# Kernel optimization log

Measured on AMD Instinct MI355X. Metric: run time of the kernel, lower is better.

## Reference

```python
import jax, jax.numpy as jnp
import numpy as np

EPS = 1e-08  # attention offset, matches module epsilon


def _ln(x, g, b, eps=1e-5):
    m = jnp.mean(x, axis=-1, keepdims=True)
    v = jnp.var(x, axis=-1, keepdims=True)
    return (x - m) * jax.lax.rsqrt(v + eps) * g + b


def setup_inputs() -> dict:
    key = jax.random.key(0)
    ks = jax.random.split(key, 12)
    B, N, D, S, H = 32, 16384, 64, 7, 128
    sc = 1.0 / np.sqrt(D)
    sch = 1.0 / np.sqrt(H)
    return {
        "inputs": jax.random.normal(ks[0], (B, N, D), jnp.float32),
        "ln_in_g": jnp.ones((D,), jnp.float32), "ln_in_b": jnp.zeros((D,), jnp.float32),
        "ln_slots_g": jnp.ones((D,), jnp.float32), "ln_slots_b": jnp.zeros((D,), jnp.float32),
        "ln_mlp_g": jnp.ones((D,), jnp.float32), "ln_mlp_b": jnp.zeros((D,), jnp.float32),
        "Wq": jax.random.normal(ks[1], (D, D), jnp.float32) * sc,
        "Wk": jax.random.normal(ks[2], (D, D), jnp.float32) * sc,
        "Wv": jax.random.normal(ks[3], (D, D), jnp.float32) * sc,
        "slots_mu": jax.random.normal(ks[4], (1, 1, D), jnp.float32),
        "slots_log_sigma": jax.random.normal(ks[5], (1, 1, D), jnp.float32) * 0.1,
        "w_ih": jax.random.normal(ks[6], (3 * D, D), jnp.float32) * sc,
        "w_hh": jax.random.normal(ks[7], (3 * D, D), jnp.float32) * sc,
        "b_ih": jnp.zeros((3 * D,), jnp.float32), "b_hh": jnp.zeros((3 * D,), jnp.float32),
        "mlp_w1": jax.random.normal(ks[8], (H, D), jnp.float32) * sc,
        "mlp_b1": jnp.zeros((H,), jnp.float32),
        "mlp_w2": jax.random.normal(ks[9], (D, H), jnp.float32) * sch,
        "mlp_b2": jnp.zeros((D,), jnp.float32),
        "noise_slots": jax.random.normal(ks[10], (B, S, D), jnp.float32),
        "noise_h": jax.random.normal(ks[11], (B, D), jnp.float32),
        "num_iterations": 3,
    }


def reference(inputs, ln_in_g, ln_in_b, ln_slots_g, ln_slots_b, ln_mlp_g, ln_mlp_b,
              Wq, Wk, Wv, slots_mu, slots_log_sigma, w_ih, w_hh, b_ih, b_hh,
              mlp_w1, mlp_b1, mlp_w2, mlp_b2, noise_slots, noise_h, num_iterations):
    D = inputs.shape[-1]
    scale = D ** -0.5

    x = _ln(inputs, ln_in_g, ln_in_b)               # [B,N,D]
    k = jnp.einsum('bnd,ed->bne', x, Wk)            # [B,N,D]
    v = jnp.einsum('bnd,ed->bne', x, Wv)            # [B,N,D]

    sigma = jnp.exp(slots_log_sigma)
    slots = slots_mu + sigma * noise_slots          # [B,S,D]
    h0 = (slots_mu + sigma * noise_h[None])[0]      # [B,D] (torch h0 is [1,B,D])

    def gru_step(h, x_t):  # torch GRU cell, gate order r,z,n
        gi = x_t @ w_ih.T + b_ih
        gh = h @ w_hh.T + b_hh
        ir, iz, inn = jnp.split(gi, 3, axis=-1)
        hr, hz, hn = jnp.split(gh, 3, axis=-1)
        r = jax.nn.sigmoid(ir + hr)
        z = jax.nn.sigmoid(iz + hz)
        n = jnp.tanh(inn + r * hn)
        h_new = (1.0 - z) * n + z * h
        return h_new, h_new

    for _ in range(num_iterations):
        sn = _ln(slots, ln_slots_g, ln_slots_b)
        q = jnp.einsum('bsd,ed->bse', sn, Wq) * scale        # [B,S,D]
        logits = jnp.einsum('bnd,bsd->bns', k, q)            # [B,N,S]
        attn = jax.nn.softmax(logits, axis=-1) + EPS          # softmax over slots
        attn = attn / jnp.sum(attn, axis=1, keepdims=True)   # normalize over inputs (dim=-2)
        updates = jnp.einsum('bns,bnd->bsd', attn, v)        # [B,S,D]
        # nn.GRU over the slot axis as "time", fixed h0 each iteration
        _, hs = jax.lax.scan(gru_step, h0, jnp.swapaxes(updates, 0, 1))
        slots = jnp.swapaxes(hs, 0, 1)                       # [B,S,D]
        hid = jax.nn.relu(_ln(slots, ln_mlp_g, ln_mlp_b) @ mlp_w1.T + mlp_b1)
        slots = slots + (hid @ mlp_w2.T + mlp_b2)
    return slots
```

## Files before the change

### kernel.cpp

```cpp
#include <hip/hip_runtime.h>
#include <hip/hip_bf16.h>


#define B_ 32
#define N_ 16384
#define D_ 64
#define S_ 7

typedef __bf16 bf16x8 __attribute__((ext_vector_type(8)));
typedef float floatx4 __attribute__((ext_vector_type(4)));

__device__ __forceinline__ unsigned int f2bfu(float f) {
  __hip_bfloat16 h = __float2bfloat16(f);
  return (unsigned int)__builtin_bit_cast(unsigned short, h);
}
__device__ __forceinline__ unsigned int pack2bf(float lo, float hi) {
  return f2bfu(lo) | (f2bfu(hi) << 16);
}

__device__ void q_from_slots(const float* s_slot, float* s_tmp,
                             const float* __restrict__ g, const float* __restrict__ bb,
                             const float* __restrict__ Wq, float* __restrict__ qout,
                             int lane, int w)
{
  for (int ss = 0; ss < 2; ++ss) {
    int srow = ss * 4 + w;
    if (srow < 7) {
      float xv = s_slot[srow * 64 + lane];
      float s1 = xv, s2 = xv * xv;
#pragma unroll
      for (int mm = 1; mm < 64; mm <<= 1) {
        s1 += __shfl_xor(s1, mm);
        s2 += __shfl_xor(s2, mm);
      }
      float mean = s1 * 0.015625f;
      float var = s2 * 0.015625f - mean * mean;
      float rs = rsqrtf(var + 1e-5f);
      s_tmp[w * 64 + lane] = (xv - mean) * rs * g[lane] + bb[lane];
    }
    __syncthreads();
    if (srow < 7) {
      float acc = 0.f;
      const float4* wr = (const float4*)(Wq + lane * 64);
      const float4* xr = (const float4*)(s_tmp + w * 64);
#pragma unroll
      for (int i = 0; i < 16; ++i) {
        float4 a = wr[i], xx = xr[i];
        acc += a.x * xx.x + a.y * xx.y + a.z * xx.z + a.w * xx.w;
      }
      qout[srow * 64 + lane] = acc * 0.125f;
    }
    __syncthreads();
  }
}

__global__ __launch_bounds__(256) void init_kernel(
    const float* __restrict__ mu, const float* __restrict__ lsig,
    const float* __restrict__ nslots, const float* __restrict__ nh,
    const float* __restrict__ ln_s_g, const float* __restrict__ ln_s_b,
    const float* __restrict__ Wq,
    const float* __restrict__ Wk, const float* __restrict__ Wv,
    float* __restrict__ qbuf, float* __restrict__ h0b,
    unsigned short* __restrict__ wkb, unsigned short* __restrict__ wvb)
{
  __shared__ float s_slot[448];
  __shared__ float s_tmp[256];
  const int b = blockIdx.x, t = threadIdx.x, lane = t & 63, w = t >> 6;
  {
    int gid = b * 256 + t;
    if (gid < 4096) wkb[gid] = (unsigned short)f2bfu(Wk[gid]);
    else            wvb[gid - 4096] = (unsigned short)f2bfu(Wv[gid - 4096]);
  }
  for (int o = t; o < 448; o += 256) {
    int d = o & 63;
    s_slot[o] = mu[d] + expf(lsig[d]) * nslots[b * 448 + o];
  }
  if (t < 64) h0b[b * 64 + t] = mu[t] + expf(lsig[t]) * nh[b * 64 + t];
  __syncthreads();
  q_from_slots(s_slot, s_tmp, ln_s_g, ln_s_b, Wq, qbuf + b * 448, lane, w);
}

__global__ __launch_bounds__(256, 4) void proj_kernel(
    const float* __restrict__ x,
    const float* __restrict__ lng, const float* __restrict__ lnb,
    const unsigned short* __restrict__ wkb, const unsigned short* __restrict__ wvb,
    const float* __restrict__ qbuf,
    unsigned short* __restrict__ kb, unsigned short* __restrict__ vt,
    float* __restrict__ Wp, float* __restrict__ Cp)
{
  __shared__ __align__(16) unsigned char smemA[18432];
  __shared__ __align__(16) unsigned short s_vo[64 * 136];
  __shared__ __align__(16) unsigned short s_qb[1024];
  __shared__ float s_cred[4][8];
  unsigned short* s_xn = (unsigned short*)smemA;
  unsigned short* s_ko = (unsigned short*)smemA;
  unsigned short* s_at = (unsigned short*)smemA;
  float* s_red = (float*)(smemA + 5120);

  const int t = threadIdx.x, lane = t & 63, w = t >> 6;
  const int R0 = blockIdx.x * 128;
  const int bb = R0 >> 14;
  const int tile = blockIdx.x;

  {
    int i0 = t * 4;
    int s = i0 >> 6, d0 = i0 & 63;
    float f0 = 0.f, f1 = 0.f, f2 = 0.f, f3 = 0.f;
    if (s < 7) {
      const float* qp = qbuf + bb * 448 + s * 64 + d0;
      f0 = qp[0]; f1 = qp[1]; f2 = qp[2]; f3 = qp[3];
    }
    uint2 p;
    p.x = pack2bf(f0, f1);
    p.y = pack2bf(f2, f3);
    *(uint2*)&s_qb[i0] = p;
  }

  const int ql = t & 3;
  float4 g4[4], b4[4];
#pragma unroll
  for (int j = 0; j < 4; ++j) {
    g4[j] = *(const float4*)&lng[ql * 16 + j * 4];
    b4[j] = *(const float4*)&lnb[ql * 16 + j * 4];
  }
#pragma unroll
  for (int half = 0; half < 2; ++half) {
    int r = half * 64 + (t >> 2);
    const float4* xp = (const float4*)&x[(size_t)(R0 + r) * 64 + ql * 16];
    float4 xv[4];
#pragma unroll
    for (int j = 0; j < 4; ++j) xv[j] = xp[j];
    float s1 = 0.f, s2 = 0.f;
#pragma unroll
    for (int j = 0; j < 4; ++j) {
      s1 += xv[j].x + xv[j].y + xv[j].z + xv[j].w;
      s2 += xv[j].x * xv[j].x + xv[j].y * xv[j].y + xv[j].z * xv[j].z + xv[j].w * xv[j].w;
    }
    s1 += __shfl_xor(s1, 1); s2 += __shfl_xor(s2, 1);
    s1 += __shfl_xor(s1, 2); s2 += __shfl_xor(s2, 2);
    float mean = s1 * 0.015625f;
    float var = s2 * 0.015625f - mean * mean;
    float rs = rsqrtf(var + 1e-5f);
    float y[16];
#pragma unroll
    for (int j = 0; j < 4; ++j) {
      y[j * 4 + 0] = (xv[j].x - mean) * rs * g4[j].x + b4[j].x;
      y[j * 4 + 1] = (xv[j].y - mean) * rs * g4[j].y + b4[j].y;
      y[j * 4 + 2] = (xv[j].z - mean) * rs * g4[j].z + b4[j].z;
      y[j * 4 + 3] = (xv[j].w - mean) * rs * g4[j].w + b4[j].w;
    }
#pragma unroll
    for (int h = 0; h < 2; ++h) {
      uint4 p;
      p.x = pack2bf(y[h * 8 + 0], y[h * 8 + 1]);
      p.y = pack2bf(y[h * 8 + 2], y[h * 8 + 3]);
      p.z = pack2bf(y[h * 8 + 4], y[h * 8 + 5]);
      p.w = pack2bf(y[h * 8 + 6], y[h * 8 + 7]);
      int c = ql * 2 + h;
      int sc = c ^ (r & 7);
      *(uint4*)&s_xn[r * 64 + sc * 8] = p;
    }
  }
  __syncthreads();

  const int m16 = lane & 15, quad = lane >> 4;
  bf16x8 bq0 = *(const bf16x8*)&s_qb[m16 * 64 + quad * 8];
  bf16x8 bq1 = *(const bf16x8*)&s_qb[m16 * 64 + 32 + quad * 8];

  bf16x8 bf[2][2];
#pragma unroll
  for (int rt = 0; rt < 2; ++rt) {
    int xr = (w * 2 + rt) * 16 + m16;
#pragma unroll
    for (int kk = 0; kk < 2; ++kk)
      bf[rt][kk] = *(const bf16x8*)&s_xn[xr * 64 + (((kk * 4 + quad) ^ (xr & 7)) * 8)];
  }
  bf16x8 wkf[4][2], wvf[4][2];
#pragma unroll
  for (int ft = 0; ft < 4; ++ft)
#pragma unroll
    for (int kk = 0; kk < 2; ++kk) {
      wkf[ft][kk] = *(const bf16x8*)&wkb[(ft * 16 + m16) * 64 + kk * 32 + quad * 8];
      wvf[ft][kk] = *(const bf16x8*)&wvb[(ft * 16 + m16) * 64 + kk * 32 + quad * 8];
    }
  __syncthreads();

#pragma unroll
  for (int ft = 0; ft < 4; ++ft)
#pragma unroll
    for (int rt = 0; rt < 2; ++rt) {
      floatx4 acc = (floatx4){0.f, 0.f, 0.f, 0.f};
      acc = __builtin_amdgcn_mfma_f32_16x16x32_bf16(wkf[ft][0], bf[rt][0], acc, 0, 0, 0);
      acc = __builtin_amdgcn_mfma_f32_16x16x32_bf16(wkf[ft][1], bf[rt][1], acc, 0, 0, 0);
      int n_l = (w * 2 + rt) * 16 + m16;
      uint2 p;
      p.x = pack2bf(acc[0], acc[1]);
      p.y = pack2bf(acc[2], acc[3]);
      *(uint2*)&s_ko[n_l * 72 + ft * 16 + quad * 4] = p;
    }
  __syncthreads();

#pragma unroll
  for (int ft = 0; ft < 4; ++ft)
#pragma unroll
    for (int rt = 0; rt < 2; ++rt) {
      floatx4 acc = (floatx4){0.f, 0.f, 0.f, 0.f};
      acc = __builtin_amdgcn_mfma_f32_16x16x32_bf16(bf[rt][0], wvf[ft][0], acc, 0, 0, 0);
      acc = __builtin_amdgcn_mfma_f32_16x16x32_bf16(bf[rt][1], wvf[ft][1], acc, 0, 0, 0);
      int n_l = (w * 2 + rt) * 16 + quad * 4;
      int d0 = ft * 16 + m16;
      uint2 p;
      p.x = pack2bf(acc[0], acc[1]);
      p.y = pack2bf(acc[2], acc[3]);
      *(uint2*)&s_vo[d0 * 136 + n_l] = p;
    }
  bf16x8 ak[2][2];
#pragma unroll
  for (int rt = 0; rt < 2; ++rt) {
    int row = (w * 2 + rt) * 16 + m16;
    ak[rt][0] = *(const bf16x8*)&s_ko[row * 72 + quad * 8];
    ak[rt][1] = *(const bf16x8*)&s_ko[row * 72 + 32 + quad * 8];
  }
#pragma unroll
  for (int p = 0; p < 4; ++p) {
    int ii = (p * 256 + t) * 8;
    int n_l = ii >> 6, dl = ii & 63;
    uint4 v4 = *(const uint4*)&s_ko[n_l * 72 + dl];
    *(uint4*)&kb[(size_t)(R0 + n_l) * 64 + dl] = v4;
  }
  __syncthreads();

  float cl = 0.f;
#pragma unroll
  for (int rt = 0; rt < 2; ++rt) {
    floatx4 c = (floatx4){0.f, 0.f, 0.f, 0.f};
    c = __builtin_amdgcn_mfma_f32_16x16x32_bf16(ak[rt][0], bq0, c, 0, 0, 0);
    c = __builtin_amdgcn_mfma_f32_16x16x32_bf16(ak[rt][1], bq1, c, 0, 0, 0);
    float atv[4];
#pragma unroll
    for (int rg = 0; rg < 4; ++rg) {
      float e = (m16 < 7) ? __expf(c[rg]) : 0.f;
      float sm = e;
      sm += __shfl_xor(sm, 1);
      sm += __shfl_xor(sm, 2);
      sm += __shfl_xor(sm, 4);
      float a = e * __builtin_amdgcn_rcpf(sm) + 1e-8f;
      atv[rg] = a;
      cl += a;
    }
    if (m16 < 7) {
      uint2 p;
      p.x = pack2bf(atv[0], atv[1]);
      p.y = pack2bf(atv[2], atv[3]);
      *(uint2*)&s_at[w * 640 + m16 * 40 + rt * 16 + quad * 4] = p;
    }
  }
  asm volatile("s_waitcnt lgkmcnt(0)" ::: "memory");
  bf16x8 af = *(const bf16x8*)&s_at[w * 640 + m16 * 40 + quad * 8];
  floatx4 acc2[4];
#pragma unroll
  for (int dt = 0; dt < 4; ++dt) acc2[dt] = (floatx4){0.f, 0.f, 0.f, 0.f};
#pragma unroll
  for (int dt = 0; dt < 4; ++dt) {
    bf16x8 bv = *(const bf16x8*)&s_vo[(dt * 16 + m16) * 136 + w * 32 + quad * 8];
    acc2[dt] = __builtin_amdgcn_mfma_f32_16x16x32_bf16(af, bv, acc2[dt], 0, 0, 0);
  }
  if (quad < 2) {
#pragma unroll
    for (int dt = 0; dt < 4; ++dt)
#pragma unroll
      for (int rg = 0; rg < 4; ++rg) {
        int s = quad * 4 + rg;
        if (s < 7) s_red[w * 448 + s * 64 + dt * 16 + m16] = acc2[dt][rg];
      }
  }
  cl += __shfl_xor(cl, 16);
  cl += __shfl_xor(cl, 32);
  if (m16 < 7 && quad == 0) s_cred[w][m16] = cl;
  __syncthreads();

  for (int o = t; o < 448; o += 256) {
    float v = s_red[o] + s_red[448 + o] + s_red[896 + o] + s_red[1344 + o];
    Wp[(size_t)tile * 448 + o] = v;
  }
  if (t < 7) {
    float c = s_cred[0][t] + s_cred[1][t] + s_cred[2][t] + s_cred[3][t];
    Cp[(size_t)tile * 8 + t] = c;
  }
#pragma unroll
  for (int p = 0; p < 4; ++p) {
    int ii = (p * 256 + t) * 8;
    int d0 = ii >> 7, nl = ii & 127;
    uint4 v4 = *(const uint4*)&s_vo[d0 * 136 + nl];
    *(uint4*)&vt[(size_t)tile * 8192 + ii] = v4;
  }
}

__global__ __launch_bounds__(256, 4) void attn_kernel(
    const unsigned short* __restrict__ kb, const unsigned short* __restrict__ vt,
    const float* __restrict__ qbuf,
    float* __restrict__ Wp, float* __restrict__ Cp)
{
  __shared__ __align__(16) unsigned short s_qb[16 * 64];
  __shared__ __align__(16) unsigned short s_at[4][16 * 72];
  __shared__ __align__(16) float s_red[4][448];
  __shared__ float s_cred[4][8];

  const int b = blockIdx.y;
  const int t = threadIdx.x, lane = t & 63, w = t >> 6;
  const int m16 = lane & 15, quad = lane >> 4;

  {
    int i0 = t * 4;
    int s = i0 >> 6, d0 = i0 & 63;
    float f0 = 0.f, f1 = 0.f, f2 = 0.f, f3 = 0.f;
    if (s < 7) {
      const float* qp = qbuf + b * 448 + s * 64 + d0;
      f0 = qp[0]; f1 = qp[1]; f2 = qp[2]; f3 = qp[3];
    }
    uint2 p;
    p.x = pack2bf(f0, f1);
    p.y = pack2bf(f2, f3);
    *(uint2*)&s_qb[i0] = p;
  }
  __syncthreads();

  bf16x8 bq0 = *(const bf16x8*)&s_qb[m16 * 64 + quad * 8];
  bf16x8 bq1 = *(const bf16x8*)&s_qb[m16 * 64 + 32 + quad * 8];

  const int n0w = blockIdx.x * 256 + w * 64;
  const unsigned short* kbA = kb + ((size_t)b * N_ + n0w) * 64;

  bf16x8 ak[4][2];
#pragma unroll
  for (int nt = 0; nt < 4; ++nt) {
    ak[nt][0] = *(const bf16x8*)&kbA[(size_t)(nt * 16 + m16) * 64 + quad * 8];
    ak[nt][1] = *(const bf16x8*)&kbA[(size_t)(nt * 16 + m16) * 64 + 32 + quad * 8];
  }
  floatx4 cc[4];
#pragma unroll
  for (int nt = 0; nt < 4; ++nt) {
    floatx4 c = (floatx4){0.f, 0.f, 0.f, 0.f};
    c = __builtin_amdgcn_mfma_f32_16x16x32_bf16(ak[nt][0], bq0, c, 0, 0, 0);
    c = __builtin_amdgcn_mfma_f32_16x16x32_bf16(ak[nt][1], bq1, c, 0, 0, 0);
    cc[nt] = c;
  }
  float cl = 0.f;
#pragma unroll
  for (int nt = 0; nt < 4; ++nt) {
    float atv[4];
#pragma unroll
    for (int rg = 0; rg < 4; ++rg) {
      float e = (m16 < 7) ? __expf(cc[nt][rg]) : 0.f;
      float sm = e;
      sm += __shfl_xor(sm, 1);
      sm += __shfl_xor(sm, 2);
      sm += __shfl_xor(sm, 4);
      float a = e * __builtin_amdgcn_rcpf(sm) + 1e-8f;
      atv[rg] = a;
      cl += a;
    }
    if (m16 < 7) {
      uint2 p;
      p.x = pack2bf(atv[0], atv[1]);
      p.y = pack2bf(atv[2], atv[3]);
      *(uint2*)&s_at[w][m16 * 72 + nt * 16 + quad * 4] = p;
    }
  }

  bf16x8 bv[2][4];
  const unsigned short* vtB = vt + (size_t)(b * 128 + (n0w >> 7)) * 8192 + (n0w & 127);
#pragma unroll
  for (int ch = 0; ch < 2; ++ch)
#pragma unroll
    for (int dt = 0; dt < 4; ++dt)
      bv[ch][dt] = *(const bf16x8*)&vtB[(dt * 16 + m16) * 128 + ch * 32 + quad * 8];
  asm volatile("s_waitcnt lgkmcnt(0)" ::: "memory");
  bf16x8 af0 = *(const bf16x8*)&s_at[w][m16 * 72 + quad * 8];
  bf16x8 af1 = *(const bf16x8*)&s_at[w][m16 * 72 + 32 + quad * 8];

  floatx4 acc[4];
#pragma unroll
  for (int dt = 0; dt < 4; ++dt) acc[dt] = (floatx4){0.f, 0.f, 0.f, 0.f};
#pragma unroll
  for (int dt = 0; dt < 4; ++dt)
    acc[dt] = __builtin_amdgcn_mfma_f32_16x16x32_bf16(af0, bv[0][dt], acc[dt], 0, 0, 0);
#pragma unroll
  for (int dt = 0; dt < 4; ++dt)
    acc[dt] = __builtin_amdgcn_mfma_f32_16x16x32_bf16(af1, bv[1][dt], acc[dt], 0, 0, 0);

  if (quad < 2) {
#pragma unroll
    for (int dt = 0; dt < 4; ++dt)
#pragma unroll
      for (int rg = 0; rg < 4; ++rg) {
        int s = quad * 4 + rg;
        if (s < 7) s_red[w][s * 64 + dt * 16 + m16] = acc[dt][rg];
      }
  }
  cl += __shfl_xor(cl, 16);
  cl += __shfl_xor(cl, 32);
  if (m16 < 7 && quad == 0) s_cred[w][m16] = cl;
  __syncthreads();

  for (int o = t; o < 448; o += 256) {
    float v = s_red[0][o] + s_red[1][o] + s_red[2][o] + s_red[3][o];
    Wp[((size_t)b * 64 + blockIdx.x) * 448 + o] = v;
  }
  if (t < 7) {
    float c = s_cred[0][t] + s_cred[1][t] + s_cred[2][t] + s_cred[3][t];
    Cp[((size_t)b * 64 + blockIdx.x) * 8 + t] = c;
  }
}

__global__ __launch_bounds__(512) void slot_update_kernel(
    const float* __restrict__ Wp, const float* __restrict__ Cp, int npart,
    const float* __restrict__ h0b,
    const float* __restrict__ w_ih, const float* __restrict__ w_hh,
    const float* __restrict__ b_ih, const float* __restrict__ b_hh,
    const float* __restrict__ ln_m_g, const float* __restrict__ ln_m_b,
    const float* __restrict__ w1, const float* __restrict__ b1,
    const float* __restrict__ w2, const float* __restrict__ b2,
    const float* __restrict__ ln_s_g, const float* __restrict__ ln_s_b,
    const float* __restrict__ Wq,
    float* __restrict__ qbuf, float* __restrict__ out, int flags)
{
  const int b = blockIdx.x, t = threadIdx.x, lane = t & 63, w = t >> 6;
  __shared__ float s_whhT[64 * 201];
  __shared__ float s_upd[448];
  __shared__ float s_gi[1344];
  __shared__ float s_slot[448];
  __shared__ float s_tmp[512];
  __shared__ float s_cs[8];

  for (int i = t; i < 12288; i += 512) {
    int j = i >> 6, d = i & 63;
    s_whhT[d * 201 + j] = w_hh[i];
  }
  if (t < 7) {
    float cs = 0.f;
#pragma unroll 8
    for (int p = 0; p < npart; ++p) cs += Cp[((size_t)b * npart + p) * 8 + t];
    s_cs[t] = cs;
  }
  __syncthreads();
  if (t < 448) {
    float acc = 0.f;
#pragma unroll 8
    for (int p = 0; p < npart; ++p) acc += Wp[((size_t)b * npart + p) * 448 + t];
    s_upd[t] = acc / s_cs[t >> 6];
  }
  __syncthreads();
  for (int o = t; o < 1344; o += 512) {
    int s = o / 192, j = o - s * 192;
    float acc = b_ih[j];
    const float4* wr = (const float4*)(w_ih + j * 64);
    const float4* ur = (const float4*)(s_upd + s * 64);
#pragma unroll
    for (int i = 0; i < 16; ++i) {
      float4 a = wr[i], u = ur[i];
      acc += a.x * u.x + a.y * u.y + a.z * u.z + a.w * u.w;
    }
    s_gi[o] = acc;
  }
  __syncthreads();
  if (w == 0) {
    float h = h0b[b * 64 + lane];
    const float bhr = b_hh[lane], bhz = b_hh[64 + lane], bhn = b_hh[128 + lane];
    const float* wr_ = &s_whhT[lane];
    const float* wz_ = &s_whhT[64 + lane];
    const float* wn_ = &s_whhT[128 + lane];
    for (int s = 0; s < 7; ++s) {
      float ar = bhr, az = bhz, an = bhn;
#pragma unroll 8
      for (int d = 0; d < 64; ++d) {
        float hd = __shfl(h, d);
        ar += hd * wr_[d * 201];
        az += hd * wz_[d * 201];
        an += hd * wn_[d * 201];
      }
      float ir = s_gi[s * 192 + lane], iz = s_gi[s * 192 + 64 + lane], inn = s_gi[s * 192 + 128 + lane];
      float r = 1.f / (1.f + __expf(-(ir + ar)));
      float z = 1.f / (1.f + __expf(-(iz + az)));
      float n = tanhf(inn + r * an);
      h = (1.f - z) * n + z * h;
      s_slot[s * 64 + lane] = h;
    }
  }
  __syncthreads();
  float* s_sn = s_gi;
  float* s_hid = s_gi + 448;
  if (w < 7) {
    float xv = s_slot[w * 64 + lane];
    float s1 = xv, s2 = xv * xv;
#pragma unroll
    for (int mm = 1; mm < 64; mm <<= 1) {
      s1 += __shfl_xor(s1, mm);
      s2 += __shfl_xor(s2, mm);
    }
    float mean = s1 * 0.015625f;
    float var = s2 * 0.015625f - mean * mean;
    float rs = rsqrtf(var + 1e-5f);
    s_sn[w * 64 + lane] = (xv - mean) * rs * ln_m_g[lane] + ln_m_b[lane];
  }
  __syncthreads();
  for (int o = t; o < 896; o += 512) {
    int s = o >> 7, hh = o & 127;
    float acc = b1[hh];
    const float4* wr = (const float4*)(w1 + hh * 64);
    const float4* xr = (const float4*)(s_sn + s * 64);
#pragma unroll
    for (int i = 0; i < 16; ++i) {
      float4 a = wr[i], xx = xr[i];
      acc += a.x * xx.x + a.y * xx.y + a.z * xx.z + a.w * xx.w;
    }
    s_hid[o] = fmaxf(acc, 0.f);
  }
  __syncthreads();
  for (int o = t; o < 448; o += 512) {
    int s = o >> 6, d = o & 63;
    float acc = b2[d];
    const float4* wr = (const float4*)(w2 + d * 128);
    const float4* hr = (const float4*)(s_hid + s * 128);
#pragma unroll
    for (int i = 0; i < 32; ++i) {
      float4 a = wr[i], hv = hr[i];
      acc += a.x * hv.x + a.y * hv.y + a.z * hv.z + a.w * hv.w;
    }
    float val = s_slot[o] + acc;
    s_slot[o] = val;
    if (flags & 1) out[b * 448 + o] = val;
  }
  __syncthreads();
  if (flags & 2) {
    if (w < 7) {
      float xv = s_slot[w * 64 + lane];
      float s1 = xv, s2 = xv * xv;
#pragma unroll
      for (int mm = 1; mm < 64; mm <<= 1) {
        s1 += __shfl_xor(s1, mm);
        s2 += __shfl_xor(s2, mm);
      }
      float mean = s1 * 0.015625f;
      float var = s2 * 0.015625f - mean * mean;
      float rs = rsqrtf(var + 1e-5f);
      s_tmp[w * 64 + lane] = (xv - mean) * rs * ln_s_g[lane] + ln_s_b[lane];
    }
    __syncthreads();
    if (w < 7) {
      float acc = 0.f;
      const float4* wr = (const float4*)(Wq + lane * 64);
      const float4* xr = (const float4*)(s_tmp + w * 64);
#pragma unroll
      for (int i = 0; i < 16; ++i) {
        float4 a = wr[i], xx = xr[i];
        acc += a.x * xx.x + a.y * xx.y + a.z * xx.z + a.w * xx.w;
      }
      qbuf[b * 448 + w * 64 + lane] = acc * 0.125f;
    }
  }
}

extern "C" void kernel_launch(void* const* d_in, const int* in_sizes, int n_in,
                              void* d_out, int out_size, void* d_ws, size_t ws_size,
                              hipStream_t stream)
{
  (void)in_sizes; (void)n_in; (void)out_size; (void)ws_size;
  const float* x      = (const float*)d_in[0];
  const float* ln_in_g = (const float*)d_in[1];
  const float* ln_in_b = (const float*)d_in[2];
  const float* ln_s_g  = (const float*)d_in[3];
  const float* ln_s_b  = (const float*)d_in[4];
  const float* ln_m_g  = (const float*)d_in[5];
  const float* ln_m_b  = (const float*)d_in[6];
  const float* Wq = (const float*)d_in[7];
  const float* Wk = (const float*)d_in[8];
  const float* Wv = (const float*)d_in[9];
  const float* mu = (const float*)d_in[10];
  const float* lsig = (const float*)d_in[11];
  const float* w_ih = (const float*)d_in[12];
  const float* w_hh = (const float*)d_in[13];
  const float* b_ih = (const float*)d_in[14];
  const float* b_hh = (const float*)d_in[15];
  const float* w1 = (const float*)d_in[16];
  const float* b1 = (const float*)d_in[17];
  const float* w2 = (const float*)d_in[18];
  const float* b2 = (const float*)d_in[19];
  const float* nslots = (const float*)d_in[20];
  const float* nh = (const float*)d_in[21];

  unsigned short* kb  = (unsigned short*)d_ws;
  unsigned short* vt  = kb + (size_t)B_ * N_ * D_;
  unsigned short* wkb = vt + (size_t)B_ * N_ * D_;
  unsigned short* wvb = wkb + 4096;
  float* fb  = (float*)(wvb + 4096);
  float* qbuf = fb;
  float* h0b  = fb + 14336;
  float* Wp   = fb + 16384;
  float* Cp   = Wp + 1835008;
  float* out = (float*)d_out;

  init_kernel<<<32, 256, 0, stream>>>(mu, lsig, nslots, nh, ln_s_g, ln_s_b, Wq,
                                      Wk, Wv, qbuf, h0b, wkb, wvb);
  proj_kernel<<<4096, 256, 0, stream>>>(x, ln_in_g, ln_in_b, wkb, wvb, qbuf, kb, vt, Wp, Cp);
  slot_update_kernel<<<32, 512, 0, stream>>>(Wp, Cp, 128, h0b, w_ih, w_hh, b_ih, b_hh,
                                             ln_m_g, ln_m_b, w1, b1, w2, b2,
                                             ln_s_g, ln_s_b, Wq, qbuf, out, 2);
  attn_kernel<<<dim3(64, 32), 256, 0, stream>>>(kb, vt, qbuf, Wp, Cp);
  slot_update_kernel<<<32, 512, 0, stream>>>(Wp, Cp, 64, h0b, w_ih, w_hh, b_ih, b_hh,
                                             ln_m_g, ln_m_b, w1, b1, w2, b2,
                                             ln_s_g, ln_s_b, Wq, qbuf, out, 2);
  attn_kernel<<<dim3(64, 32), 256, 0, stream>>>(kb, vt, qbuf, Wp, Cp);
  slot_update_kernel<<<32, 512, 0, stream>>>(Wp, Cp, 64, h0b, w_ih, w_hh, b_ih, b_hh,
                                             ln_m_g, ln_m_b, w1, b1, w2, b2,
                                             ln_s_g, ln_s_b, Wq, qbuf, out, 1);
}
```

Before: 449.5 us.

## Fuse iterations 2-3 attention and slot updates into one per-batch persistent kernel

Replaces the separate attention and slot-update launches for the later iterations with a single kernel that uses one 1024-thread block per batch. Each block streams its batch's K and V tiles, computes attention with MFMA, reduces in shared memory and runs the GRU and MLP update in place, keeping q in shared memory. The GRU hidden-weight product now reads w_hh directly from global memory instead of staging a transpose in LDS. This removes launch and global round-trip overhead but restricts the bandwidth-heavy attention passes to only 32 workgroups.

```diff
diff --git a/kernel.cpp b/kernel.cpp
--- a/kernel.cpp
+++ b/kernel.cpp
@@ -84,7 +84,7 @@
     const float* __restrict__ x,
     const float* __restrict__ lng, const float* __restrict__ lnb,
     const unsigned short* __restrict__ wkb, const unsigned short* __restrict__ wvb,
-    const float* __restrict__ qbuf,
+    const float* __restrict__ qin,
     unsigned short* __restrict__ kb, unsigned short* __restrict__ vt,
     float* __restrict__ Wp, float* __restrict__ Cp)
 {
@@ -107,7 +107,7 @@
     int s = i0 >> 6, d0 = i0 & 63;
     float f0 = 0.f, f1 = 0.f, f2 = 0.f, f3 = 0.f;
     if (s < 7) {
-      const float* qp = qbuf + bb * 448 + s * 64 + d0;
+      const float* qp = qin + bb * 448 + s * 64 + d0;
       f0 = qp[0]; f1 = qp[1]; f2 = qp[2]; f3 = qp[3];
     }
     uint2 p;
@@ -290,131 +290,14 @@
 #pragma unroll
   for (int p = 0; p < 4; ++p) {
     int ii = (p * 256 + t) * 8;
-    int d0 = ii >> 7, nl = ii & 127;
-    uint4 v4 = *(const uint4*)&s_vo[d0 * 136 + nl];
+    uint4 v4 = *(const uint4*)&s_vo[(ii >> 7) * 136 + (ii & 127)];
     *(uint4*)&vt[(size_t)tile * 8192 + ii] = v4;
   }
 }
 
-__global__ __launch_bounds__(256, 4) void attn_kernel(
-    const unsigned short* __restrict__ kb, const unsigned short* __restrict__ vt,
-    const float* __restrict__ qbuf,
-    float* __restrict__ Wp, float* __restrict__ Cp)
-{
-  __shared__ __align__(16) unsigned short s_qb[16 * 64];
-  __shared__ __align__(16) unsigned short s_at[4][16 * 72];
-  __shared__ __align__(16) float s_red[4][448];
-  __shared__ float s_cred[4][8];
-
-  const int b = blockIdx.y;
-  const int t = threadIdx.x, lane = t & 63, w = t >> 6;
-  const int m16 = lane & 15, quad = lane >> 4;
-
-  {
-    int i0 = t * 4;
-    int s = i0 >> 6, d0 = i0 & 63;
-    float f0 = 0.f, f1 = 0.f, f2 = 0.f, f3 = 0.f;
-    if (s < 7) {
-      const float* qp = qbuf + b * 448 + s * 64 + d0;
-      f0 = qp[0]; f1 = qp[1]; f2 = qp[2]; f3 = qp[3];
-    }
-    uint2 p;
-    p.x = pack2bf(f0, f1);
-    p.y = pack2bf(f2, f3);
-    *(uint2*)&s_qb[i0] = p;
-  }
-  __syncthreads();
-
-  bf16x8 bq0 = *(const bf16x8*)&s_qb[m16 * 64 + quad * 8];
-  bf16x8 bq1 = *(const bf16x8*)&s_qb[m16 * 64 + 32 + quad * 8];
-
-  const int n0w = blockIdx.x * 256 + w * 64;
-  const unsigned short* kbA = kb + ((size_t)b * N_ + n0w) * 64;
-
-  bf16x8 ak[4][2];
-#pragma unroll
-  for (int nt = 0; nt < 4; ++nt) {
-    ak[nt][0] = *(const bf16x8*)&kbA[(size_t)(nt * 16 + m16) * 64 + quad * 8];
-    ak[nt][1] = *(const bf16x8*)&kbA[(size_t)(nt * 16 + m16) * 64 + 32 + quad * 8];
-  }
-  floatx4 cc[4];
-#pragma unroll
-  for (int nt = 0; nt < 4; ++nt) {
-    floatx4 c = (floatx4){0.f, 0.f, 0.f, 0.f};
-    c = __builtin_amdgcn_mfma_f32_16x16x32_bf16(ak[nt][0], bq0, c, 0, 0, 0);
-    c = __builtin_amdgcn_mfma_f32_16x16x32_bf16(ak[nt][1], bq1, c, 0, 0, 0);
-    cc[nt] = c;
-  }
-  float cl = 0.f;
-#pragma unroll
-  for (int nt = 0; nt < 4; ++nt) {
-    float atv[4];
-#pragma unroll
-    for (int rg = 0; rg < 4; ++rg) {
-      float e = (m16 < 7) ? __expf(cc[nt][rg]) : 0.f;
-      float sm = e;
-      sm += __shfl_xor(sm, 1);
-      sm += __shfl_xor(sm, 2);
-      sm += __shfl_xor(sm, 4);
-      float a = e * __builtin_amdgcn_rcpf(sm) + 1e-8f;
-      atv[rg] = a;
-      cl += a;
-    }
-    if (m16 < 7) {
-      uint2 p;
-      p.x = pack2bf(atv[0], atv[1]);
-      p.y = pack2bf(atv[2], atv[3]);
-      *(uint2*)&s_at[w][m16 * 72 + nt * 16 + quad * 4] = p;
-    }
-  }
-
-  bf16x8 bv[2][4];
-  const unsigned short* vtB = vt + (size_t)(b * 128 + (n0w >> 7)) * 8192 + (n0w & 127);
-#pragma unroll
-  for (int ch = 0; ch < 2; ++ch)
-#pragma unroll
-    for (int dt = 0; dt < 4; ++dt)
-      bv[ch][dt] = *(const bf16x8*)&vtB[(dt * 16 + m16) * 128 + ch * 32 + quad * 8];
-  asm volatile("s_waitcnt lgkmcnt(0)" ::: "memory");
-  bf16x8 af0 = *(const bf16x8*)&s_at[w][m16 * 72 + quad * 8];
-  bf16x8 af1 = *(const bf16x8*)&s_at[w][m16 * 72 + 32 + quad * 8];
-
-  floatx4 acc[4];
-#pragma unroll
-  for (int dt = 0; dt < 4; ++dt) acc[dt] = (floatx4){0.f, 0.f, 0.f, 0.f};
-#pragma unroll
-  for (int dt = 0; dt < 4; ++dt)
-    acc[dt] = __builtin_amdgcn_mfma_f32_16x16x32_bf16(af0, bv[0][dt], acc[dt], 0, 0, 0);
-#pragma unroll
-  for (int dt = 0; dt < 4; ++dt)
-    acc[dt] = __builtin_amdgcn_mfma_f32_16x16x32_bf16(af1, bv[1][dt], acc[dt], 0, 0, 0);
-
-  if (quad < 2) {
-#pragma unroll
-    for (int dt = 0; dt < 4; ++dt)
-#pragma unroll
-      for (int rg = 0; rg < 4; ++rg) {
-        int s = quad * 4 + rg;
-        if (s < 7) s_red[w][s * 64 + dt * 16 + m16] = acc[dt][rg];
-      }
-  }
-  cl += __shfl_xor(cl, 16);
-  cl += __shfl_xor(cl, 32);
-  if (m16 < 7 && quad == 0) s_cred[w][m16] = cl;
-  __syncthreads();
-
-  for (int o = t; o < 448; o += 256) {
-    float v = s_red[0][o] + s_red[1][o] + s_red[2][o] + s_red[3][o];
-    Wp[((size_t)b * 64 + blockIdx.x) * 448 + o] = v;
-  }
-  if (t < 7) {
-    float c = s_cred[0][t] + s_cred[1][t] + s_cred[2][t] + s_cred[3][t];
-    Cp[((size_t)b * 64 + blockIdx.x) * 8 + t] = c;
-  }
-}
-
-__global__ __launch_bounds__(512) void slot_update_kernel(
-    const float* __restrict__ Wp, const float* __restrict__ Cp, int npart,
+__device__ void slot_core_1024(
+    int b, int t, int lane, int w,
+    float* s_upd, float* s_gi, float* s_slot, unsigned short* s_qb,
     const float* __restrict__ h0b,
     const float* __restrict__ w_ih, const float* __restrict__ w_hh,
     const float* __restrict__ b_ih, const float* __restrict__ b_hh,
@@ -423,35 +306,10 @@
     const float* __restrict__ w2, const float* __restrict__ b2,
     const float* __restrict__ ln_s_g, const float* __restrict__ ln_s_b,
     const float* __restrict__ Wq,
-    float* __restrict__ qbuf, float* __restrict__ out, int flags)
+    float* __restrict__ out, int flags)
 {
-  const int b = blockIdx.x, t = threadIdx.x, lane = t & 63, w = t >> 6;
-  __shared__ float s_whhT[64 * 201];
-  __shared__ float s_upd[448];
-  __shared__ float s_gi[1344];
-  __shared__ float s_slot[448];
-  __shared__ float s_tmp[512];
-  __shared__ float s_cs[8];
-
-  for (int i = t; i < 12288; i += 512) {
-    int j = i >> 6, d = i & 63;
-    s_whhT[d * 201 + j] = w_hh[i];
-  }
-  if (t < 7) {
-    float cs = 0.f;
-#pragma unroll 8
-    for (int p = 0; p < npart; ++p) cs += Cp[((size_t)b * npart + p) * 8 + t];
-    s_cs[t] = cs;
-  }
-  __syncthreads();
-  if (t < 448) {
-    float acc = 0.f;
-#pragma unroll 8
-    for (int p = 0; p < npart; ++p) acc += Wp[((size_t)b * npart + p) * 448 + t];
-    s_upd[t] = acc / s_cs[t >> 6];
-  }
-  __syncthreads();
-  for (int o = t; o < 1344; o += 512) {
+  __syncthreads();
+  for (int o = t; o < 1344; o += 1024) {
     int s = o / 192, j = o - s * 192;
     float acc = b_ih[j];
     const float4* wr = (const float4*)(w_ih + j * 64);
@@ -467,17 +325,19 @@
   if (w == 0) {
     float h = h0b[b * 64 + lane];
     const float bhr = b_hh[lane], bhz = b_hh[64 + lane], bhn = b_hh[128 + lane];
-    const float* wr_ = &s_whhT[lane];
-    const float* wz_ = &s_whhT[64 + lane];
-    const float* wn_ = &s_whhT[128 + lane];
+    const float4* wr4 = (const float4*)(w_hh + lane * 64);
+    const float4* wz4 = (const float4*)(w_hh + (64 + lane) * 64);
+    const float4* wn4 = (const float4*)(w_hh + (128 + lane) * 64);
     for (int s = 0; s < 7; ++s) {
       float ar = bhr, az = bhz, an = bhn;
-#pragma unroll 8
-      for (int d = 0; d < 64; ++d) {
-        float hd = __shfl(h, d);
-        ar += hd * wr_[d * 201];
-        az += hd * wz_[d * 201];
-        an += hd * wn_[d * 201];
+#pragma unroll
+      for (int i = 0; i < 16; ++i) {
+        float4 a = wr4[i], zz = wz4[i], c = wn4[i];
+        float h0 = __shfl(h, i * 4 + 0), h1 = __shfl(h, i * 4 + 1);
+        float h2 = __shfl(h, i * 4 + 2), h3 = __shfl(h, i * 4 + 3);
+        ar += a.x * h0 + a.y * h1 + a.z * h2 + a.w * h3;
+        az += zz.x * h0 + zz.y * h1 + zz.z * h2 + zz.w * h3;
+        an += c.x * h0 + c.y * h1 + c.z * h2 + c.w * h3;
       }
       float ir = s_gi[s * 192 + lane], iz = s_gi[s * 192 + 64 + lane], inn = s_gi[s * 192 + 128 + lane];
       float r = 1.f / (1.f + __expf(-(ir + ar)));
@@ -504,7 +364,7 @@
     s_sn[w * 64 + lane] = (xv - mean) * rs * ln_m_g[lane] + ln_m_b[lane];
   }
   __syncthreads();
-  for (int o = t; o < 896; o += 512) {
+  for (int o = t; o < 896; o += 1024) {
     int s = o >> 7, hh = o & 127;
     float acc = b1[hh];
     const float4* wr = (const float4*)(w1 + hh * 64);
@@ -517,7 +377,7 @@
     s_hid[o] = fmaxf(acc, 0.f);
   }
   __syncthreads();
-  for (int o = t; o < 448; o += 512) {
+  for (int o = t; o < 448; o += 1024) {
     int s = o >> 6, d = o & 63;
     float acc = b2[d];
     const float4* wr = (const float4*)(w2 + d * 128);
@@ -544,20 +404,164 @@
       float mean = s1 * 0.015625f;
       float var = s2 * 0.015625f - mean * mean;
       float rs = rsqrtf(var + 1e-5f);
-      s_tmp[w * 64 + lane] = (xv - mean) * rs * ln_s_g[lane] + ln_s_b[lane];
+      s_upd[w * 64 + lane] = (xv - mean) * rs * ln_s_g[lane] + ln_s_b[lane];
     }
     __syncthreads();
     if (w < 7) {
       float acc = 0.f;
       const float4* wr = (const float4*)(Wq + lane * 64);
-      const float4* xr = (const float4*)(s_tmp + w * 64);
+      const float4* xr = (const float4*)(s_upd + w * 64);
 #pragma unroll
       for (int i = 0; i < 16; ++i) {
         float4 a = wr[i], xx = xr[i];
         acc += a.x * xx.x + a.y * xx.y + a.z * xx.z + a.w * xx.w;
       }
-      qbuf[b * 448 + w * 64 + lane] = acc * 0.125f;
-    }
+      s_qb[w * 64 + lane] = (unsigned short)f2bfu(acc * 0.125f);
+    }
+  }
+}
+
+__global__ __launch_bounds__(1024) void iter23_kernel(
+    const unsigned short* __restrict__ kb, const unsigned short* __restrict__ vt,
+    const float* __restrict__ Wp, const float* __restrict__ Cp,
+    const float* __restrict__ h0b,
+    const float* __restrict__ w_ih, const float* __restrict__ w_hh,
+    const float* __restrict__ b_ih, const float* __restrict__ b_hh,
+    const float* __restrict__ ln_m_g, const float* __restrict__ ln_m_b,
+    const float* __restrict__ w1, const float* __restrict__ b1,
+    const float* __restrict__ w2, const float* __restrict__ b2,
+    const float* __restrict__ ln_s_g, const float* __restrict__ ln_s_b,
+    const float* __restrict__ Wq,
+    float* __restrict__ out)
+{
+  __shared__ __align__(16) unsigned short s_qb[1024];
+  __shared__ __align__(16) unsigned short s_at[16][1152];
+  __shared__ __align__(16) float s_red[16][448];
+  __shared__ float s_cred[16][8];
+  __shared__ float s_upd[448];
+  __shared__ float s_gi[1344];
+  __shared__ float s_slot[448];
+  __shared__ float s_cs[8];
+
+  const int b = blockIdx.x;
+  const int t = threadIdx.x, lane = t & 63, w = t >> 6;
+  const int m16 = lane & 15, quad = lane >> 4;
+
+  s_qb[t] = 0;
+
+  {
+    if (t < 7) {
+      float cs = 0.f;
+#pragma unroll 8
+      for (int p = 0; p < 128; ++p) cs += Cp[((size_t)b * 128 + p) * 8 + t];
+      s_cs[t] = cs;
+    }
+    float num = 0.f;
+    if (t < 448) {
+#pragma unroll 8
+      for (int p = 0; p < 128; ++p) num += Wp[((size_t)b * 128 + p) * 448 + t];
+    }
+    __syncthreads();
+    if (t < 448) s_upd[t] = num / s_cs[t >> 6];
+    slot_core_1024(b, t, lane, w, s_upd, s_gi, s_slot, s_qb,
+                   h0b, w_ih, w_hh, b_ih, b_hh, ln_m_g, ln_m_b,
+                   w1, b1, w2, b2, ln_s_g, ln_s_b, Wq, out, 2);
+  }
+
+  const unsigned short* kbA = kb + ((size_t)b * N_ + w * 1024) * 64;
+  for (int it = 0; it < 2; ++it) {
+    __syncthreads();
+    bf16x8 bq0 = *(const bf16x8*)&s_qb[m16 * 64 + quad * 8];
+    bf16x8 bq1 = *(const bf16x8*)&s_qb[m16 * 64 + 32 + quad * 8];
+
+    floatx4 acc[4];
+#pragma unroll
+    for (int dt = 0; dt < 4; ++dt) acc[dt] = (floatx4){0.f, 0.f, 0.f, 0.f};
+    float cl = 0.f;
+
+    for (int c = 0; c < 16; ++c) {
+      bf16x8 ak0[4], ak1[4];
+#pragma unroll
+      for (int nt = 0; nt < 4; ++nt) {
+        const unsigned short* kr = kbA + (size_t)(c * 64 + nt * 16 + m16) * 64;
+        ak0[nt] = *(const bf16x8*)&kr[quad * 8];
+        ak1[nt] = *(const bf16x8*)&kr[32 + quad * 8];
+      }
+#pragma unroll
+      for (int nt = 0; nt < 4; ++nt) {
+        floatx4 cc = (floatx4){0.f, 0.f, 0.f, 0.f};
+        cc = __builtin_amdgcn_mfma_f32_16x16x32_bf16(ak0[nt], bq0, cc, 0, 0, 0);
+        cc = __builtin_amdgcn_mfma_f32_16x16x32_bf16(ak1[nt], bq1, cc, 0, 0, 0);
+        float atv[4];
+#pragma unroll
+        for (int rg = 0; rg < 4; ++rg) {
+          float e = (m16 < 7) ? __expf(cc[rg]) : 0.f;
+          float sm = e;
+          sm += __shfl_xor(sm, 1);
+          sm += __shfl_xor(sm, 2);
+          sm += __shfl_xor(sm, 4);
+          float a = e * __builtin_amdgcn_rcpf(sm) + 1e-8f;
+          atv[rg] = a;
+          cl += a;
+        }
+        if (m16 < 7) {
+          uint2 p;
+          p.x = pack2bf(atv[0], atv[1]);
+          p.y = pack2bf(atv[2], atv[3]);
+          *(uint2*)&s_at[w][m16 * 72 + nt * 16 + quad * 4] = p;
+        }
+      }
+      asm volatile("s_waitcnt lgkmcnt(0)" ::: "memory");
+      bf16x8 af0 = *(const bf16x8*)&s_at[w][m16 * 72 + quad * 8];
+      bf16x8 af1 = *(const bf16x8*)&s_at[w][m16 * 72 + 32 + quad * 8];
+      const int R = w * 1024 + c * 64;
+      const unsigned short* vtB = vt + ((size_t)b * 128 + (R >> 7)) * 8192 + (R & 127);
+#pragma unroll
+      for (int ch = 0; ch < 2; ++ch) {
+        bf16x8 bv[4];
+#pragma unroll
+        for (int dt = 0; dt < 4; ++dt)
+          bv[dt] = *(const bf16x8*)&vtB[(dt * 16 + m16) * 128 + ch * 32 + quad * 8];
+        bf16x8 af = (ch == 0) ? af0 : af1;
+#pragma unroll
+        for (int dt = 0; dt < 4; ++dt)
+          acc[dt] = __builtin_amdgcn_mfma_f32_16x16x32_bf16(af, bv[dt], acc[dt], 0, 0, 0);
+      }
+    }
+
+    if (quad < 2) {
+#pragma unroll
+      for (int dt = 0; dt < 4; ++dt)
+#pragma unroll
+        for (int rg = 0; rg < 4; ++rg) {
+          int s = quad * 4 + rg;
+          if (s < 7) s_red[w][s * 64 + dt * 16 + m16] = acc[dt][rg];
+        }
+    }
+    cl += __shfl_xor(cl, 16);
+    cl += __shfl_xor(cl, 32);
+    if (m16 < 7 && quad == 0) s_cred[w][m16] = cl;
+    __syncthreads();
+
+    float num = 0.f;
+    if (t < 448) {
+#pragma unroll
+      for (int wv = 0; wv < 16; ++wv) num += s_red[wv][t];
+    }
+    if (t >= 512 && t < 519) {
+      int s = t - 512;
+      float c = 0.f;
+#pragma unroll
+      for (int wv = 0; wv < 16; ++wv) c += s_cred[wv][s];
+      s_cs[s] = c;
+    }
+    __syncthreads();
+    if (t < 448) s_upd[t] = num / s_cs[t >> 6];
+
+    slot_core_1024(b, t, lane, w, s_upd, s_gi, s_slot, s_qb,
+                   h0b, w_ih, w_hh, b_ih, b_hh, ln_m_g, ln_m_b,
+                   w1, b1, w2, b2, ln_s_g, ln_s_b, Wq, out,
+                   (it == 1) ? 1 : 2);
   }
 }
 
@@ -594,24 +598,17 @@
   unsigned short* wkb = vt + (size_t)B_ * N_ * D_;
   unsigned short* wvb = wkb + 4096;
   float* fb  = (float*)(wvb + 4096);
-  float* qbuf = fb;
-  float* h0b  = fb + 14336;
-  float* Wp   = fb + 16384;
-  float* Cp   = Wp + 1835008;
+  float* qbuf0 = fb;
+  float* h0b   = fb + 14336;
+  float* Wp    = fb + 16384;
+  float* Cp    = Wp + 1835008;
   float* out = (float*)d_out;
 
   init_kernel<<<32, 256, 0, stream>>>(mu, lsig, nslots, nh, ln_s_g, ln_s_b, Wq,
-                                      Wk, Wv, qbuf, h0b, wkb, wvb);
-  proj_kernel<<<4096, 256, 0, stream>>>(x, ln_in_g, ln_in_b, wkb, wvb, qbuf, kb, vt, Wp, Cp);
-  slot_update_kernel<<<32, 512, 0, stream>>>(Wp, Cp, 128, h0b, w_ih, w_hh, b_ih, b_hh,
-                                             ln_m_g, ln_m_b, w1, b1, w2, b2,
-                                             ln_s_g, ln_s_b, Wq, qbuf, out, 2);
-  attn_kernel<<<dim3(64, 32), 256, 0, stream>>>(kb, vt, qbuf, Wp, Cp);
-  slot_update_kernel<<<32, 512, 0, stream>>>(Wp, Cp, 64, h0b, w_ih, w_hh, b_ih, b_hh,
-                                             ln_m_g, ln_m_b, w1, b1, w2, b2,
-                                             ln_s_g, ln_s_b, Wq, qbuf, out, 2);
-  attn_kernel<<<dim3(64, 32), 256, 0, stream>>>(kb, vt, qbuf, Wp, Cp);
-  slot_update_kernel<<<32, 512, 0, stream>>>(Wp, Cp, 64, h0b, w_ih, w_hh, b_ih, b_hh,
-                                             ln_m_g, ln_m_b, w1, b1, w2, b2,
-                                             ln_s_g, ln_s_b, Wq, qbuf, out, 1);
-}
+                                      Wk, Wv, qbuf0, h0b, wkb, wvb);
+  proj_kernel<<<4096, 256, 0, stream>>>(x, ln_in_g, ln_in_b, wkb, wvb, qbuf0,
+                                        kb, vt, Wp, Cp);
+  iter23_kernel<<<32, 1024, 0, stream>>>(kb, vt, Wp, Cp,
+                                         h0b, w_ih, w_hh, b_ih, b_hh, ln_m_g, ln_m_b,
+                                         w1, b1, w2, b2, ln_s_g, ln_s_b, Wq, out);
+}
```

Result: slower. 779.0 us (+73.3%).
